# Kernel optimization log

Measured on AMD Instinct MI355X. Metric: run time of the kernel, lower is better.

Reference implementation:

```python
import jax, jax.numpy as jnp
import numpy as np

H = 12      # num_attention_heads
DM = 768    # hidden_size
HD = DM // H  # head_dim = 64


def setup_inputs() -> dict:
    key = jax.random.key(0)
    ks = jax.random.split(key, 9)
    B, L = 4, 2048
    s = 0.02
    return {
        "hidden_states": jax.random.normal(ks[0], (B, L, DM), jnp.float32),
        "wq": jax.random.normal(ks[1], (DM, DM), jnp.float32) * s,
        "bq": jnp.zeros((DM,), jnp.float32),
        "wk": jax.random.normal(ks[2], (DM, DM), jnp.float32) * s,
        "bk": jnp.zeros((DM,), jnp.float32),
        "wv": jax.random.normal(ks[3], (DM, DM), jnp.float32) * s,
        "bv": jnp.zeros((DM,), jnp.float32),
        "wo": jax.random.normal(ks[4], (DM, DM), jnp.float32) * s,
        "bo": jnp.zeros((DM,), jnp.float32),
    }


def reference(hidden_states, wq, bq, wk, bk, wv, bv, wo, bo):
    B, L, D = hidden_states.shape
    scale = HD ** -0.5
    # torch Linear: x @ W.T + b
    q = hidden_states @ wq.T + bq
    k = hidden_states @ wk.T + bk
    v = hidden_states @ wv.T + bv
    # [B, H, L, HD]
    q = q.reshape(B, L, H, HD).transpose(0, 2, 1, 3)
    k = k.reshape(B, L, H, HD).transpose(0, 2, 1, 3)
    v = v.reshape(B, L, H, HD).transpose(0, 2, 1, 3)
    attn = jnp.einsum('bhqd,bhkd->bhqk', q, k) * scale
    causal = jnp.tril(jnp.ones((L, L), dtype=bool))
    attn = jnp.where(causal, attn, jnp.float32(-jnp.inf))
    attn = jax.nn.softmax(attn, axis=-1)
    out = jnp.einsum('bhqk,bhkd->bhqd', attn, v)
    out = out.transpose(0, 2, 1, 3).reshape(B, L, D)
    return out @ wo.T + bo
```

## Files before the change

kernel.cpp:

```cpp
#include <hip/hip_runtime.h>

typedef unsigned short ushort_t;
typedef __attribute__((ext_vector_type(8))) short short8;
typedef __attribute__((ext_vector_type(4))) float f32x4;

__device__ __forceinline__ ushort_t f2b(float f) {
    union { float f; unsigned int i; } v; v.f = f;
    unsigned int x = v.i;
    return (ushort_t)((x + 0x7fffu + ((x >> 16) & 1u)) >> 16);
}
__device__ __forceinline__ ushort_t f2b_fast(float f) {
    union { float f; unsigned int i; } v; v.f = f;
    return (ushort_t)((v.i + 0x8000u) >> 16);
}
__device__ __forceinline__ float exp2_hw(float x) {
    return __builtin_amdgcn_exp2f(x);
}
__device__ __forceinline__ void dma16(const ushort_t* g, ushort_t* l) {
    __builtin_amdgcn_global_load_lds(
        (const __attribute__((address_space(1))) unsigned int*)g,
        (__attribute__((address_space(3))) unsigned int*)l, 16, 0, 0);
}

__global__ __launch_bounds__(256)
void convert_bf16(const float* __restrict__ hs, const float* __restrict__ wq,
                  const float* __restrict__ wk, const float* __restrict__ wv,
                  const float* __restrict__ wo,
                  ushort_t* __restrict__ hsb, ushort_t* __restrict__ wqb,
                  ushort_t* __restrict__ wkb, ushort_t* __restrict__ wvb,
                  ushort_t* __restrict__ wob)
{
    const int y = blockIdx.y;
    const float* src; ushort_t* dst; int n;
    if (y == 0)      { src = hs; dst = hsb; n = 8192 * 768; }
    else if (y == 1) { src = wq; dst = wqb; n = 768 * 768; }
    else if (y == 2) { src = wk; dst = wkb; n = 768 * 768; }
    else if (y == 3) { src = wv; dst = wvb; n = 768 * 768; }
    else             { src = wo; dst = wob; n = 768 * 768; }
    const int idx = (blockIdx.x * 256 + threadIdx.x) * 8;
    if (idx >= n) return;
    const float4 a = ((const float4*)(src + idx))[0];
    const float4 b = ((const float4*)(src + idx))[1];
    ushort_t tmp[8] = { f2b(a.x), f2b(a.y), f2b(a.z), f2b(a.w),
                        f2b(b.x), f2b(b.y), f2b(b.z), f2b(b.w) };
    *(uint4*)(dst + idx) = *(const uint4*)tmp;
}

#define NIT 24

template<int MODE>
__global__ __launch_bounds__(256, 3)
void gemm_mfma(const ushort_t* __restrict__ A,
               const ushort_t* __restrict__ W0, const ushort_t* __restrict__ W1,
               const ushort_t* __restrict__ W2,
               const float* __restrict__ b0, const float* __restrict__ b1,
               const float* __restrict__ b2,
               void* __restrict__ C0, void* __restrict__ C1, void* __restrict__ C2)
{
    __shared__ __attribute__((aligned(16))) ushort_t Ab[3][128 * 32];
    __shared__ __attribute__((aligned(16))) ushort_t Wb[3][128 * 32];

    const int id   = blockIdx.x;
    const int xcd  = id & 7;
    const int slot = id >> 3;
    int mtile, otile, z;
    if (MODE == 0) {
        mtile = (slot / 18) * 8 + xcd;
        const int rem = slot % 18;
        otile = rem % 6;
        z     = rem / 6;
    } else {
        mtile = (slot / 6) * 8 + xcd;
        otile = slot % 6;
        z     = 0;
    }
    const ushort_t* W = (z == 0) ? W0 : (z == 1) ? W1 : W2;
    const float* bias  = (z == 0) ? b0 : (z == 1) ? b1 : b2;
    void* C            = (z == 0) ? C0 : (z == 1) ? C1 : C2;

    const int t    = threadIdx.x;
    const int lane = t & 63;
    const int w    = t >> 6;
    const int col  = lane & 15;
    const int kg   = lane >> 4;
    const int m0   = mtile * 128;
    const int o0   = otile * 128;
    const int mh   = (w & 1) * 64;
    const int oh   = (w >> 1) * 64;

    f32x4 acc[4][4];
#pragma unroll
    for (int mt = 0; mt < 4; ++mt)
#pragma unroll
        for (int nt = 0; nt < 4; ++nt) acc[mt][nt] = (f32x4){0.f, 0.f, 0.f, 0.f};

    const int lrow = lane >> 2;
    const int lgr  = (lane & 3) ^ ((lane >> 3) & 3);
    const ushort_t* pa = A + (size_t)(m0 + lrow) * 768 + lgr * 8;
    const ushort_t* pw = W + (size_t)(o0 + lrow) * 768 + lgr * 8;

    auto stage = [&](int c, int b) {
#pragma unroll
        for (int j = 0; j < 2; ++j) {
            const int q = 2 * w + j;
            dma16(pa + (size_t)q * (16 * 768) + c * 32, &Ab[b][q * 512]);
            dma16(pw + (size_t)q * (16 * 768) + c * 32, &Wb[b][q * 512]);
        }
    };

    const int gq = (kg ^ ((col >> 1) & 3)) * 8;

    auto step = [&](int it, int cur, int nb) {
        __builtin_amdgcn_s_barrier();
        if (it + 2 < NIT) {
            stage(it + 2, nb);
            asm volatile("s_waitcnt vmcnt(8)" ::: "memory");
        } else if (it + 1 < NIT) {
            asm volatile("s_waitcnt vmcnt(4)" ::: "memory");
        } else {
            asm volatile("s_waitcnt vmcnt(0)" ::: "memory");
        }
        __builtin_amdgcn_sched_barrier(0);

        short8 wf[4], af[4];
#pragma unroll
        for (int nt = 0; nt < 4; ++nt)
            wf[nt] = *(const short8*)&Wb[cur][(oh + nt * 16 + col) * 32 + gq];
#pragma unroll
        for (int mt = 0; mt < 4; ++mt)
            af[mt] = *(const short8*)&Ab[cur][(mh + mt * 16 + col) * 32 + gq];

#pragma unroll
        for (int mt = 0; mt < 4; ++mt)
#pragma unroll
            for (int nt = 0; nt < 4; ++nt)
                acc[mt][nt] = __builtin_amdgcn_mfma_f32_16x16x32_bf16(
                    af[mt], wf[nt], acc[mt][nt], 0, 0, 0);
    };

    stage(0, 0);
    stage(1, 1);
    for (int j = 0; j < NIT; j += 3) {
        step(j + 0, 0, 2);
        step(j + 1, 1, 0);
        step(j + 2, 2, 1);
    }

    float bias_v[4];
#pragma unroll
    for (int nt = 0; nt < 4; ++nt) bias_v[nt] = bias[o0 + oh + nt * 16 + col];
    const float scale = (MODE == 0 && z == 0) ? 0.18033688011112042f : 1.0f;

#pragma unroll
    for (int mt = 0; mt < 4; ++mt)
#pragma unroll
        for (int nt = 0; nt < 4; ++nt) {
            const int mb = m0 + mh + mt * 16 + kg * 4;
            const int o  = o0 + oh + nt * 16 + col;
            if (MODE == 0 && z == 2) {
                ushort_t tmp[4];
#pragma unroll
                for (int r = 0; r < 4; ++r) tmp[r] = f2b(acc[mt][nt][r] + bias_v[nt]);
                const size_t dst = ((size_t)((mb >> 11) * 12 + (o >> 6)) << 17)
                                 + ((size_t)(o & 63) << 11) + (mb & 2047);
                *(uint2*)((ushort_t*)C + dst) = *(const uint2*)tmp;
            } else {
#pragma unroll
                for (int r = 0; r < 4; ++r) {
                    const int m = mb + r;
                    const float v = (acc[mt][nt][r] + bias_v[nt]) * scale;
                    if (MODE == 0) {
                        const size_t dst = ((size_t)((m >> 11) * 12 + (o >> 6)) << 17)
                                         + ((size_t)(m & 2047) << 6) + (o & 63);
                        ((ushort_t*)C)[dst] = f2b(v);
                    } else {
                        ((float*)C)[(size_t)m * 768 + o] = v;
                    }
                }
            }
        }
}

#define KV_STRIDE 72

struct pafrag { short8 a0, a1; };

__device__ __forceinline__ pafrag p_redist(f32x4 s0, f32x4 s1, f32x4 s2,
                                           f32x4 s3, int kg)
{
    unsigned int P2[4][2];
    asm("v_cvt_pk_bf16_f32 %0, %1, %2" : "=v"(P2[0][0]) : "v"(s0[0]), "v"(s0[1]));
    asm("v_cvt_pk_bf16_f32 %0, %1, %2" : "=v"(P2[0][1]) : "v"(s0[2]), "v"(s0[3]));
    asm("v_cvt_pk_bf16_f32 %0, %1, %2" : "=v"(P2[1][0]) : "v"(s1[0]), "v"(s1[1]));
    asm("v_cvt_pk_bf16_f32 %0, %1, %2" : "=v"(P2[1][1]) : "v"(s1[2]), "v"(s1[3]));
    asm("v_cvt_pk_bf16_f32 %0, %1, %2" : "=v"(P2[2][0]) : "v"(s2[0]), "v"(s2[1]));
    asm("v_cvt_pk_bf16_f32 %0, %1, %2" : "=v"(P2[2][1]) : "v"(s2[2]), "v"(s2[3]));
    asm("v_cvt_pk_bf16_f32 %0, %1, %2" : "=v"(P2[3][0]) : "v"(s3[0]), "v"(s3[1]));
    asm("v_cvt_pk_bf16_f32 %0, %1, %2" : "=v"(P2[3][1]) : "v"(s3[2]), "v"(s3[3]));
    const bool klo = (kg < 2);
    unsigned int X16[4], X32[4];
    X16[0] = klo ? P2[0][0] : P2[1][0];
    X16[1] = klo ? P2[0][1] : P2[1][1];
    X16[2] = klo ? P2[2][0] : P2[3][0];
    X16[3] = klo ? P2[2][1] : P2[3][1];
    X32[0] = klo ? P2[1][0] : P2[0][0];
    X32[1] = klo ? P2[1][1] : P2[0][1];
    X32[2] = klo ? P2[3][0] : P2[2][0];
    X32[3] = klo ? P2[3][1] : P2[2][1];
    unsigned int R16[4], R32[4], R48[4];
#pragma unroll
    for (int j = 0; j < 4; ++j) {
        R16[j] = (unsigned int)__shfl_xor((int)X16[j], 16);
        R32[j] = (unsigned int)__shfl_xor((int)X32[j], 32);
        R48[j] = (unsigned int)__shfl_xor((int)X32[j], 48);
    }
    unsigned int Fv[4], Sv[4];
#pragma unroll
    for (int j = 0; j < 4; ++j) {
        const unsigned int flo = (kg == 0) ? X16[j] : R48[j];
        const unsigned int fhi = (kg == 2) ? R32[j] : R16[j];
        Fv[j] = klo ? flo : fhi;
        const unsigned int slo = (kg == 0) ? R16[j] : R32[j];
        const unsigned int shi = (kg == 2) ? R48[j] : X16[j];
        Sv[j] = klo ? slo : shi;
    }
    union { unsigned int u[4]; short8 v; } A0, A1;
    A0.u[0] = Fv[0]; A0.u[1] = Fv[1]; A0.u[2] = Sv[0]; A0.u[3] = Sv[1];
    A1.u[0] = Fv[2]; A1.u[1] = Fv[3]; A1.u[2] = Sv[2]; A1.u[3] = Sv[3];
    pafrag r; r.a0 = A0.v; r.a1 = A1.v; return r;
}

__global__ __launch_bounds__(256, 3)
void attn_mfma(const ushort_t* __restrict__ Q, const ushort_t* __restrict__ K,
               const ushort_t* __restrict__ Vt, ushort_t* __restrict__ AO)
{
    __shared__ ushort_t Ks[64 * KV_STRIDE];
    __shared__ ushort_t Vs[64 * KV_STRIDE];

    const int t    = threadIdx.x;
    const int lane = t & 63;
    const int w    = t >> 6;
    const int id   = blockIdx.x;
    const int bh   = ((id >> 3) >> 4) * 8 + (id & 7);
    const int p    = (id >> 3) & 15;
    const size_t base = (size_t)bh << 17;

    const int col = lane & 15;
    const int kg  = lane >> 4;
    const int srow = t >> 2;
    const int scol = (t & 3) << 4;
    const int b = bh / 12, h = bh % 12;

    const int tileA = 31 - p;
    const int tileB = p;
    const int q0A = tileA << 6, q0B = tileB << 6;
    const int nch = tileA + 1;

    const ushort_t* pqA = Q + base + (size_t)(q0A + 16 * w + col) * 64 + kg * 8;
    const ushort_t* pqB = Q + base + (size_t)(q0B + 16 * w + col) * 64 + kg * 8;
    const short8 bqA0 = *(const short8*)pqA;
    const short8 bqA1 = *(const short8*)(pqA + 32);
    const short8 bqB0 = *(const short8*)pqB;
    const short8 bqB1 = *(const short8*)(pqB + 32);

    const int qcurA = q0A + 16 * w + col;
    const int qcurB = q0B + 16 * w + col;

    float l_runA = 0.f, l_runB = 0.f;
    f32x4 oA[4], oB[4];
#pragma unroll
    for (int vt = 0; vt < 4; ++vt) {
        oA[vt] = (f32x4){0.f, 0.f, 0.f, 0.f};
        oB[vt] = (f32x4){0.f, 0.f, 0.f, 0.f};
    }

    uint4 ka, kb, va, vb;
    {
        const ushort_t* pk = K  + base + (size_t)srow * 64 + scol;
        const ushort_t* pv = Vt + base + ((size_t)srow << 11) + scol;
        ka = *(const uint4*)pk; kb = *(const uint4*)(pk + 8);
        va = *(const uint4*)pv; vb = *(const uint4*)(pv + 8);
    }

    for (int c = 0; c < nch; ++c) {
        __syncthreads();
        *(uint4*)&Ks[srow * KV_STRIDE + scol]     = ka;
        *(uint4*)&Ks[srow * KV_STRIDE + scol + 8] = kb;
        *(uint4*)&Vs[srow * KV_STRIDE + scol]     = va;
        *(uint4*)&Vs[srow * KV_STRIDE + scol + 8] = vb;
        __syncthreads();

        if (c + 1 < nch) {
            const int k1 = (c + 1) << 6;
            const ushort_t* pk = K  + base + (size_t)(k1 + srow) * 64 + scol;
            const ushort_t* pv = Vt + base + ((size_t)srow << 11) + k1 + scol;
            ka = *(const uint4*)pk; kb = *(const uint4*)(pk + 8);
            va = *(const uint4*)pv; vb = *(const uint4*)(pv + 8);
        }

        const bool doB = (c <= tileB);

        f32x4 sA[4], sB[4];
        __builtin_amdgcn_s_setprio(1);
#pragma unroll
        for (int kt = 0; kt < 4; ++kt) {
            const ushort_t* pkf = &Ks[(kt * 16 + col) * KV_STRIDE + kg * 8];
            const short8 ak0 = *(const short8*)pkf;
            const short8 ak1 = *(const short8*)(pkf + 32);
            f32x4 a = (f32x4){0.f, 0.f, 0.f, 0.f};
            a = __builtin_amdgcn_mfma_f32_16x16x32_bf16(ak0, bqA0, a, 0, 0, 0);
            a = __builtin_amdgcn_mfma_f32_16x16x32_bf16(ak1, bqA1, a, 0, 0, 0);
            sA[kt] = a;
            if (doB) {
                f32x4 bb = (f32x4){0.f, 0.f, 0.f, 0.f};
                bb = __builtin_amdgcn_mfma_f32_16x16x32_bf16(ak0, bqB0, bb, 0, 0, 0);
                bb = __builtin_amdgcn_mfma_f32_16x16x32_bf16(ak1, bqB1, bb, 0, 0, 0);
                sB[kt] = bb;
            }
        }
        __builtin_amdgcn_s_setprio(0);

        if (c == nch - 1) {
            const int k0 = c << 6;
#pragma unroll
            for (int kt = 0; kt < 4; ++kt)
#pragma unroll
                for (int r = 0; r < 4; ++r) {
                    const int key = k0 + kt * 16 + 4 * kg + r;
                    sA[kt][r] = (key > qcurA) ? 0.f : exp2_hw(sA[kt][r]);
                }
        } else {
#pragma unroll
            for (int kt = 0; kt < 4; ++kt)
#pragma unroll
                for (int r = 0; r < 4; ++r) sA[kt][r] = exp2_hw(sA[kt][r]);
        }
#pragma unroll
        for (int kt = 0; kt < 4; ++kt)
            l_runA += (sA[kt][0] + sA[kt][1]) + (sA[kt][2] + sA[kt][3]);

        if (doB) {
            if (c == tileB) {
                const int k0 = c << 6;
#pragma unroll
                for (int kt = 0; kt < 4; ++kt)
#pragma unroll
                    for (int r = 0; r < 4; ++r) {
                        const int key = k0 + kt * 16 + 4 * kg + r;
                        sB[kt][r] = (key > qcurB) ? 0.f : exp2_hw(sB[kt][r]);
                    }
            } else {
#pragma unroll
                for (int kt = 0; kt < 4; ++kt)
#pragma unroll
                    for (int r = 0; r < 4; ++r) sB[kt][r] = exp2_hw(sB[kt][r]);
            }
#pragma unroll
            for (int kt = 0; kt < 4; ++kt)
                l_runB += (sB[kt][0] + sB[kt][1]) + (sB[kt][2] + sB[kt][3]);
        }

        pafrag pA = p_redist(sA[0], sA[1], sA[2], sA[3], kg);
        pafrag pB;
        if (doB) pB = p_redist(sB[0], sB[1], sB[2], sB[3], kg);

        __builtin_amdgcn_s_setprio(1);
#pragma unroll
        for (int vt = 0; vt < 4; ++vt) {
            const ushort_t* pvf = &Vs[(vt * 16 + col) * KV_STRIDE + kg * 8];
            const short8 v0 = *(const short8*)pvf;
            const short8 v1 = *(const short8*)(pvf + 32);
            f32x4 o = oA[vt];
            o = __builtin_amdgcn_mfma_f32_16x16x32_bf16(pA.a0, v0, o, 0, 0, 0);
            o = __builtin_amdgcn_mfma_f32_16x16x32_bf16(pA.a1, v1, o, 0, 0, 0);
            oA[vt] = o;
            if (doB) {
                f32x4 ob = oB[vt];
                ob = __builtin_amdgcn_mfma_f32_16x16x32_bf16(pB.a0, v0, ob, 0, 0, 0);
                ob = __builtin_amdgcn_mfma_f32_16x16x32_bf16(pB.a1, v1, ob, 0, 0, 0);
                oB[vt] = ob;
            }
        }
        __builtin_amdgcn_s_setprio(0);
    }

    float lsA = l_runA, lsB = l_runB;
    lsA += __shfl_xor(lsA, 16); lsA += __shfl_xor(lsA, 32);
    lsB += __shfl_xor(lsB, 16); lsB += __shfl_xor(lsB, 32);
    const float linvA = 1.f / lsA;
    const float linvB = 1.f / lsB;
    float lA4[4], lB4[4];
#pragma unroll
    for (int r = 0; r < 4; ++r) {
        lA4[r] = __shfl(linvA, 4 * kg + r);
        lB4[r] = __shfl(linvB, 4 * kg + r);
    }
#pragma unroll
    for (int vt = 0; vt < 4; ++vt)
#pragma unroll
        for (int r = 0; r < 4; ++r) {
            const int qA = q0A + 16 * w + 4 * kg + r;
            const int qB = q0B + 16 * w + 4 * kg + r;
            AO[((size_t)(b * 2048 + qA)) * 768 + h * 64 + vt * 16 + col] =
                f2b_fast(oA[vt][r] * lA4[r]);
            AO[((size_t)(b * 2048 + qB)) * 768 + h * 64 + vt * 16 + col] =
                f2b_fast(oB[vt][r] * lB4[r]);
        }
}

extern "C" void kernel_launch(void* const* d_in, const int* in_sizes, int n_in,
                              void* d_out, int out_size, void* d_ws, size_t ws_size,
                              hipStream_t stream) {
    const float* hs = (const float*)d_in[0];
    const float* wq = (const float*)d_in[1];
    const float* bq = (const float*)d_in[2];
    const float* wk = (const float*)d_in[3];
    const float* bk = (const float*)d_in[4];
    const float* wv = (const float*)d_in[5];
    const float* bv = (const float*)d_in[6];
    const float* wo = (const float*)d_in[7];
    const float* bo = (const float*)d_in[8];
    float* out = (float*)d_out;

    const size_t NB = (size_t)8192 * 768;
    const size_t WN = (size_t)768 * 768;
    ushort_t* hsb = (ushort_t*)d_ws;
    ushort_t* Qb  = hsb + NB;
    ushort_t* Kb  = Qb + NB;
    ushort_t* Vtb = Kb + NB;
    ushort_t* wqb = Vtb + NB;
    ushort_t* wkb = wqb + WN;
    ushort_t* wvb = wkb + WN;
    ushort_t* wob = wvb + WN;
    ushort_t* AO  = hsb;

    dim3 blk(256);
    convert_bf16<<<dim3(3072, 5), blk, 0, stream>>>(hs, wq, wk, wv, wo,
                                                    hsb, wqb, wkb, wvb, wob);
    gemm_mfma<0><<<dim3(1152), blk, 0, stream>>>(hsb, wqb, wkb, wvb,
                                                 bq, bk, bv, Qb, Kb, Vtb);
    attn_mfma<<<dim3(768), blk, 0, stream>>>(Qb, Kb, Vtb, AO);
    gemm_mfma<1><<<dim3(384), blk, 0, stream>>>(AO, wob, wob, wob,
                                                bo, bo, bo, out, out, out);
}
```

Before: 209.1 us.

## Triple-buffer attention K/V tiles via direct global-to-LDS DMA

The attention kernel now loads K and V chunks with global_load_lds DMA into a 3-stage LDS ring buffer, prefetching two chunks ahead. An XOR swizzle replaces the padded stride to avoid bank conflicts. This removes the register round-trip and the two __syncthreads per chunk. The GEMM step is also reordered to wait on vmcnt before the barrier and issue the next stage afterward. The change raises LDS usage to 48KB per block, which may reduce occupancy below the requested 3 blocks per CU.

```diff
diff --git a/kernel.cpp b/kernel.cpp
--- a/kernel.cpp
+++ b/kernel.cpp
@@ -111,15 +111,13 @@
     const int gq = (kg ^ ((col >> 1) & 3)) * 8;
 
     auto step = [&](int it, int cur, int nb) {
-        __builtin_amdgcn_s_barrier();
-        if (it + 2 < NIT) {
-            stage(it + 2, nb);
-            asm volatile("s_waitcnt vmcnt(8)" ::: "memory");
-        } else if (it + 1 < NIT) {
+        if (it + 1 < NIT) {
             asm volatile("s_waitcnt vmcnt(4)" ::: "memory");
         } else {
             asm volatile("s_waitcnt vmcnt(0)" ::: "memory");
         }
+        __builtin_amdgcn_s_barrier();
+        if (it + 2 < NIT) stage(it + 2, nb);
         __builtin_amdgcn_sched_barrier(0);
 
         short8 wf[4], af[4];
@@ -180,8 +178,6 @@
             }
         }
 }
-
-#define KV_STRIDE 72
 
 struct pafrag { short8 a0, a1; };
 
@@ -234,8 +230,8 @@
 void attn_mfma(const ushort_t* __restrict__ Q, const ushort_t* __restrict__ K,
                const ushort_t* __restrict__ Vt, ushort_t* __restrict__ AO)
 {
-    __shared__ ushort_t Ks[64 * KV_STRIDE];
-    __shared__ ushort_t Vs[64 * KV_STRIDE];
+    __shared__ __attribute__((aligned(16))) ushort_t Ks[3][64 * 64];
+    __shared__ __attribute__((aligned(16))) ushort_t Vs[3][64 * 64];
 
     const int t    = threadIdx.x;
     const int lane = t & 63;
@@ -247,9 +243,13 @@
 
     const int col = lane & 15;
     const int kg  = lane >> 4;
-    const int srow = t >> 2;
-    const int scol = (t & 3) << 4;
+    const int c7  = col & 7;
     const int b = bh / 12, h = bh % 12;
+
+    const int lr = lane >> 3;
+    const int lg = (lane & 7) ^ lr;
+    const ushort_t* kdma = K  + base + (size_t)lr * 64   + lg * 8;
+    const ushort_t* vdma = Vt + base + ((size_t)lr << 11) + lg * 8;
 
     const int tileA = 31 - p;
     const int tileB = p;
@@ -274,39 +274,44 @@
         oB[vt] = (f32x4){0.f, 0.f, 0.f, 0.f};
     }
 
-    uint4 ka, kb, va, vb;
-    {
-        const ushort_t* pk = K  + base + (size_t)srow * 64 + scol;
-        const ushort_t* pv = Vt + base + ((size_t)srow << 11) + scol;
-        ka = *(const uint4*)pk; kb = *(const uint4*)(pk + 8);
-        va = *(const uint4*)pv; vb = *(const uint4*)(pv + 8);
-    }
-
+    auto stageKV = [&](int c, int buf) {
+        const int k0 = c << 6;
+#pragma unroll
+        for (int j = 0; j < 2; ++j) {
+            const int qq = 2 * w + j;
+            dma16(kdma + (size_t)(k0 + qq * 8) * 64, &Ks[buf][qq * 512]);
+            dma16(vdma + ((size_t)(qq * 8) << 11) + k0, &Vs[buf][qq * 512]);
+        }
+    };
+
+    const int sk0 = (kg ^ c7) * 8;
+    const int sk1 = sk0 ^ 32;
+
+    stageKV(0, 0);
+    stageKV(1, 1);
+
+    int cur = 0, sb = 2;
     for (int c = 0; c < nch; ++c) {
-        __syncthreads();
-        *(uint4*)&Ks[srow * KV_STRIDE + scol]     = ka;
-        *(uint4*)&Ks[srow * KV_STRIDE + scol + 8] = kb;
-        *(uint4*)&Vs[srow * KV_STRIDE + scol]     = va;
-        *(uint4*)&Vs[srow * KV_STRIDE + scol + 8] = vb;
-        __syncthreads();
-
         if (c + 1 < nch) {
-            const int k1 = (c + 1) << 6;
-            const ushort_t* pk = K  + base + (size_t)(k1 + srow) * 64 + scol;
-            const ushort_t* pv = Vt + base + ((size_t)srow << 11) + k1 + scol;
-            ka = *(const uint4*)pk; kb = *(const uint4*)(pk + 8);
-            va = *(const uint4*)pv; vb = *(const uint4*)(pv + 8);
-        }
-
+            asm volatile("s_waitcnt vmcnt(4)" ::: "memory");
+        } else {
+            asm volatile("s_waitcnt vmcnt(0)" ::: "memory");
+        }
+        __builtin_amdgcn_s_barrier();
+        if (c + 2 < nch) stageKV(c + 2, sb);
+        __builtin_amdgcn_sched_barrier(0);
+
+        const ushort_t* kb = Ks[cur];
+        const ushort_t* vb = Vs[cur];
         const bool doB = (c <= tileB);
 
         f32x4 sA[4], sB[4];
         __builtin_amdgcn_s_setprio(1);
 #pragma unroll
         for (int kt = 0; kt < 4; ++kt) {
-            const ushort_t* pkf = &Ks[(kt * 16 + col) * KV_STRIDE + kg * 8];
-            const short8 ak0 = *(const short8*)pkf;
-            const short8 ak1 = *(const short8*)(pkf + 32);
+            const ushort_t* rk = &kb[(kt * 16 + col) * 64];
+            const short8 ak0 = *(const short8*)(rk + sk0);
+            const short8 ak1 = *(const short8*)(rk + sk1);
             f32x4 a = (f32x4){0.f, 0.f, 0.f, 0.f};
             a = __builtin_amdgcn_mfma_f32_16x16x32_bf16(ak0, bqA0, a, 0, 0, 0);
             a = __builtin_amdgcn_mfma_f32_16x16x32_bf16(ak1, bqA1, a, 0, 0, 0);
@@ -367,9 +372,9 @@
         __builtin_amdgcn_s_setprio(1);
 #pragma unroll
         for (int vt = 0; vt < 4; ++vt) {
-            const ushort_t* pvf = &Vs[(vt * 16 + col) * KV_STRIDE + kg * 8];
-            const short8 v0 = *(const short8*)pvf;
-            const short8 v1 = *(const short8*)(pvf + 32);
+            const ushort_t* rv = &vb[(vt * 16 + col) * 64];
+            const short8 v0 = *(const short8*)(rv + sk0);
+            const short8 v1 = *(const short8*)(rv + sk1);
             f32x4 o = oA[vt];
             o = __builtin_amdgcn_mfma_f32_16x16x32_bf16(pA.a0, v0, o, 0, 0, 0);
             o = __builtin_amdgcn_mfma_f32_16x16x32_bf16(pA.a1, v1, o, 0, 0, 0);
@@ -382,6 +387,9 @@
             }
         }
         __builtin_amdgcn_s_setprio(0);
+
+        cur = (cur == 2) ? 0 : cur + 1;
+        sb  = (sb  == 2) ? 0 : sb  + 1;
     }
 
     float lsA = l_runA, lsB = l_runB;
```

After: 211.6 us. About the same (+1.2%).

## Double M tile of QKV GEMM and move DMA wait before barrier

Applied to the files above, without the earlier changes.

The fused QKV projection GEMM now uses a 256-row M tile, so each workgroup computes 8x4 MFMA tiles per wave and half as many workgroups are launched. This reuses each staged weight tile across twice as many rows and lowers weight traffic through LDS and global memory, at the cost of more accumulator registers; launch bounds drop to 2 waves per SIMD to make room. The pipeline step now waits on its own loads (vmcnt adjusted to the per-stage load count) before the barrier and issues the next prefetch after it, so every wave's DMA for the current buffer is complete before any wave reads it.

```diff
diff --git a/kernel.cpp b/kernel.cpp
--- a/kernel.cpp
+++ b/kernel.cpp
@@ -49,7 +49,7 @@
 #define NIT 24
 
 template<int MODE>
-__global__ __launch_bounds__(256, 3)
+__global__ __launch_bounds__(256, 2)
 void gemm_mfma(const ushort_t* __restrict__ A,
                const ushort_t* __restrict__ W0, const ushort_t* __restrict__ W1,
                const ushort_t* __restrict__ W2,
@@ -57,7 +57,11 @@
                const float* __restrict__ b2,
                void* __restrict__ C0, void* __restrict__ C1, void* __restrict__ C2)
 {
-    __shared__ __attribute__((aligned(16))) ushort_t Ab[3][128 * 32];
+    constexpr int BM = (MODE == 0) ? 256 : 128;
+    constexpr int MT = BM / 32;
+    constexpr int AQ = BM / 64;
+
+    __shared__ __attribute__((aligned(16))) ushort_t Ab[3][BM * 32];
     __shared__ __attribute__((aligned(16))) ushort_t Wb[3][128 * 32];
 
     const int id   = blockIdx.x;
@@ -83,14 +87,14 @@
     const int w    = t >> 6;
     const int col  = lane & 15;
     const int kg   = lane >> 4;
-    const int m0   = mtile * 128;
+    const int m0   = mtile * BM;
     const int o0   = otile * 128;
-    const int mh   = (w & 1) * 64;
+    const int mh   = (w & 1) * (BM / 2);
     const int oh   = (w >> 1) * 64;
 
-    f32x4 acc[4][4];
-#pragma unroll
-    for (int mt = 0; mt < 4; ++mt)
+    f32x4 acc[MT][4];
+#pragma unroll
+    for (int mt = 0; mt < MT; ++mt)
 #pragma unroll
         for (int nt = 0; nt < 4; ++nt) acc[mt][nt] = (f32x4){0.f, 0.f, 0.f, 0.f};
 
@@ -101,9 +105,13 @@
 
     auto stage = [&](int c, int b) {
 #pragma unroll
+        for (int j = 0; j < AQ; ++j) {
+            const int q = AQ * w + j;
+            dma16(pa + (size_t)q * (16 * 768) + c * 32, &Ab[b][q * 512]);
+        }
+#pragma unroll
         for (int j = 0; j < 2; ++j) {
             const int q = 2 * w + j;
-            dma16(pa + (size_t)q * (16 * 768) + c * 32, &Ab[b][q * 512]);
             dma16(pw + (size_t)q * (16 * 768) + c * 32, &Wb[b][q * 512]);
         }
     };
@@ -111,27 +119,28 @@
     const int gq = (kg ^ ((col >> 1) & 3)) * 8;
 
     auto step = [&](int it, int cur, int nb) {
-        __builtin_amdgcn_s_barrier();
-        if (it + 2 < NIT) {
-            stage(it + 2, nb);
-            asm volatile("s_waitcnt vmcnt(8)" ::: "memory");
-        } else if (it + 1 < NIT) {
-            asm volatile("s_waitcnt vmcnt(4)" ::: "memory");
+        if (it + 1 < NIT) {
+            if constexpr (MODE == 0)
+                asm volatile("s_waitcnt vmcnt(6)" ::: "memory");
+            else
+                asm volatile("s_waitcnt vmcnt(4)" ::: "memory");
         } else {
             asm volatile("s_waitcnt vmcnt(0)" ::: "memory");
         }
+        __builtin_amdgcn_s_barrier();
+        if (it + 2 < NIT) stage(it + 2, nb);
         __builtin_amdgcn_sched_barrier(0);
 
-        short8 wf[4], af[4];
+        short8 wf[4], af[MT];
 #pragma unroll
         for (int nt = 0; nt < 4; ++nt)
             wf[nt] = *(const short8*)&Wb[cur][(oh + nt * 16 + col) * 32 + gq];
 #pragma unroll
-        for (int mt = 0; mt < 4; ++mt)
+        for (int mt = 0; mt < MT; ++mt)
             af[mt] = *(const short8*)&Ab[cur][(mh + mt * 16 + col) * 32 + gq];
 
 #pragma unroll
-        for (int mt = 0; mt < 4; ++mt)
+        for (int mt = 0; mt < MT; ++mt)
 #pragma unroll
             for (int nt = 0; nt < 4; ++nt)
                 acc[mt][nt] = __builtin_amdgcn_mfma_f32_16x16x32_bf16(
@@ -152,7 +161,7 @@
     const float scale = (MODE == 0 && z == 0) ? 0.18033688011112042f : 1.0f;
 
 #pragma unroll
-    for (int mt = 0; mt < 4; ++mt)
+    for (int mt = 0; mt < MT; ++mt)
 #pragma unroll
         for (int nt = 0; nt < 4; ++nt) {
             const int mb = m0 + mh + mt * 16 + kg * 4;
@@ -437,8 +446,8 @@
     dim3 blk(256);
     convert_bf16<<<dim3(3072, 5), blk, 0, stream>>>(hs, wq, wk, wv, wo,
                                                     hsb, wqb, wkb, wvb, wob);
-    gemm_mfma<0><<<dim3(1152), blk, 0, stream>>>(hsb, wqb, wkb, wvb,
-                                                 bq, bk, bv, Qb, Kb, Vtb);
+    gemm_mfma<0><<<dim3(576), blk, 0, stream>>>(hsb, wqb, wkb, wvb,
+                                                bq, bk, bv, Qb, Kb, Vtb);
     attn_mfma<<<dim3(768), blk, 0, stream>>>(Qb, Kb, Vtb, AO);
     gemm_mfma<1><<<dim3(384), blk, 0, stream>>>(AO, wob, wob, wob,
                                                 bo, bo, bo, out, out, out);
```

New measurement: 220.4 us. 5.4% more time.
